# Optimization experiments

Measured on AMD Instinct MI355X. Metric: run time of the kernel, lower is better.

## Reference

```python
import jax, jax.numpy as jnp
import numpy as np

T_STEPS = 15
THR1, THR2 = 10.0, 1.0
KWTA2, RAD2 = 8, 1


def _conv(x, w):
    # x: [T, Cin, H, W] (time steps treated as batch), w: [Cout, Cin, kh, kw]
    return jax.lax.conv_general_dilated(
        x, w, window_strides=(1, 1), padding='VALID',
        dimension_numbers=('NCHW', 'OIHW', 'NCHW'))


def _fire(pot, thr):
    # torch threshold_(pot, thr, 0): keep values strictly > thr
    tp = jnp.where(pot > thr, pot, 0.0)
    return jnp.sign(tp), tp


def _max_pool(x, k, s, p):
    return jax.lax.reduce_window(
        x, -jnp.inf, jax.lax.max,
        window_dimensions=(1, 1, k, k), window_strides=(1, 1, s, s),
        padding=((0, 0), (0, 0), (p, p), (p, p)))


def _pointwise_inhibition(tp):
    # tp: [T, C, H, W] thresholded potentials. Keep, at each (h,w), only the
    # feature with the earliest spike (ties broken by max potential).
    T = tp.shape[0]
    max_val = jnp.max(tp, axis=1, keepdims=True)          # [T,1,H,W]
    max_idx = jnp.argmax(tp, axis=1, keepdims=True)       # [T,1,H,W]
    clamp = jnp.sign(max_val)                             # [T,1,H,W]
    earliest = jnp.clip(T - clamp.sum(axis=0, keepdims=True).astype(jnp.int32),
                        0, T - 1)                          # [1,1,H,W]
    winners = jnp.take_along_axis(max_idx, earliest, axis=0)  # [1,1,H,W]
    last_sign = clamp[-1:]                                 # [1,1,H,W]
    C = tp.shape[1]
    onehot = (jnp.arange(C)[None, :, None, None] == winners).astype(tp.dtype)
    coef = onehot * last_sign                              # [1,C,H,W]
    return tp * coef


def _get_k_winners(pot, spk, kwta, radius):
    # pot, spk: [T, C, H, W]
    T, C, H, W = pot.shape
    earliest = jnp.clip(T - spk.sum(axis=0, keepdims=True).astype(jnp.int32),
                        0, T - 1)                          # [1,C,H,W]
    values = jnp.take_along_axis(pot, earliest, axis=0)    # earliest potential
    trunc = spk * values
    v = trunc.max() * T
    total = (trunc + spk * v).sum(axis=0)                  # [C,H,W]
    c_idx = jnp.arange(C)[:, None, None]
    h_idx = jnp.arange(H)[None, :, None]
    w_idx = jnp.arange(W)[None, None, :]

    def step(tot, _):
        idx = jnp.argmax(tot.reshape(-1))
        mval = tot.reshape(-1)[idx]
        valid = mval != 0
        c = idx // (H * W)
        rem = idx % (H * W)
        h = rem // W
        w = rem % W
        # suppress the winning feature everywhere + columnar inhibition window
        mask = (c_idx == c) | ((jnp.abs(h_idx - h) <= radius) &
                               (jnp.abs(w_idx - w) <= radius))
        tot = jnp.where(valid & mask, 0.0, tot)
        winner = jnp.where(valid, jnp.stack([c, h, w]).astype(jnp.int32),
                           jnp.full((3,), -1, jnp.int32))
        return tot, winner

    _, winners = jax.lax.scan(step, total, None, length=kwta)
    return winners  # [kwta, 3], -1 rows = no winner


def setup_inputs() -> dict:
    key = jax.random.key(0)
    k1, k2, k3 = jax.random.split(key, 3)
    # cumulative spike-wave: once a pixel spikes it stays 1 for later timesteps
    u = jax.random.uniform(k1, (T_STEPS, 2, 192, 192), dtype=jnp.float32)
    x = jax.lax.cummax((u < 0.05).astype(jnp.float32), axis=0)
    w1 = 0.8 + 0.05 * jax.random.normal(k2, (32, 2, 5, 5), dtype=jnp.float32)
    w2 = 0.8 + 0.05 * jax.random.normal(k3, (150, 32, 2, 2), dtype=jnp.float32)
    return {"x": x, "w1": w1, "w2": w2}


def reference(x, w1, w2):
    # training path, layer_idx != 1 (trains conv2): exercises pooling,
    # pointwise inhibition, fire, and k-winner-take-all.
    xin = jnp.pad(x, ((0, 0), (0, 0), (2, 2), (2, 2)))
    pot1 = _conv(xin, w1)                     # [T,32,192,192]
    spk1, _ = _fire(pot1, THR1)
    spk_pool = _max_pool(spk1, 2, 2, 1)       # [T,32,97,97]
    spk_in = jnp.pad(spk_pool, ((0, 0), (0, 0), (1, 1), (1, 1)))
    spk_in = _pointwise_inhibition(spk_in)
    pot2 = _conv(spk_in, w2)                  # [T,150,98,98]
    _, tp2 = _fire(pot2, THR2)
    pot = _pointwise_inhibition(tp2)
    spk = jnp.sign(pot)
    winners = _get_k_winners(pot, spk, KWTA2, RAD2)
    return pot, winners
```

## Files before the change

### kernel.cpp

```cpp
#include <hip/hip_runtime.h>

#define NT 15
#define HW1 192
#define CIN 2
#define COUT1 32
#define PH 99
#define POOL 97
#define H2 98
#define COUT2 150
#define NLOC (H2 * H2)
#define POT_ELEMS 21609000
#define N4 5402256
#define CONV1_THREADS (1152 * 256)

typedef float f32x4 __attribute__((ext_vector_type(4)));

__global__ __launch_bounds__(256) void k_first_spike(const float* __restrict__ x,
                                                     unsigned char* __restrict__ tx) {
    const int N = CIN * HW1 * HW1;
    int i = blockIdx.x * 256 + threadIdx.x;
    if (i >= N) return;
    int t = 15;
    #pragma unroll
    for (int tt = NT - 1; tt >= 0; --tt) {
        if (x[tt * N + i] > 0.5f) t = tt;
    }
    tx[i] = (unsigned char)t;
}

__global__ __launch_bounds__(256) void k_conv1(const unsigned char* __restrict__ tx,
                                               const float* __restrict__ w1,
                                               unsigned char* __restrict__ t1,
                                               f32x4* __restrict__ outfill) {
    __shared__ unsigned char stx[CIN][20][20];
    const int by = blockIdx.y * 16, bx = blockIdx.x * 16;
    const int ocg = blockIdx.z * 4;
    const int tid = threadIdx.y * 16 + threadIdx.x;

    for (int i = tid; i < CIN * 400; i += 256) {
        int ic = i / 400, rem = i % 400, r = rem / 20, c = rem % 20;
        int gy = by + r - 2, gx = bx + c - 2;
        unsigned char v = 15;
        if (gy >= 0 && gy < HW1 && gx >= 0 && gx < HW1)
            v = tx[ic * (HW1 * HW1) + gy * HW1 + gx];
        stx[ic][r][c] = v;
    }
    __syncthreads();

    {
        int bid = (blockIdx.z * 12 + blockIdx.y) * 12 + blockIdx.x;
        int g = bid * 256 + tid;
        const f32x4 z = {0.0f, 0.0f, 0.0f, 0.0f};
        for (int i = g; i < N4; i += CONV1_THREADS)
            __builtin_nontemporal_store(z, &outfill[i]);
    }

    unsigned msk[50];
    #pragma unroll
    for (int ic = 0; ic < 2; ic++)
        #pragma unroll
        for (int ky = 0; ky < 5; ky++)
            #pragma unroll
            for (int kx = 0; kx < 5; kx++)
                msk[ic * 25 + ky * 5 + kx] =
                    0xFFFFFFFFu << stx[ic][threadIdx.y + ky][threadIdx.x + kx];

    const float* wbase = w1 + ocg * 50;
    int lo[4] = {0, 0, 0, 0};
    #pragma unroll
    for (int step = 8; step >= 1; step >>= 1) {
        #pragma unroll
        for (int o = 0; o < 4; o++) {
            int mid = lo[o] + step - 1;
            float acc = 0.0f;
            #pragma unroll
            for (int q = 0; q < 50; q++) {
                float b = (float)((msk[q] >> mid) & 1u);
                acc = fmaf(wbase[o * 50 + q], b, acc);
            }
            if (!(acc > 10.0f)) lo[o] += step;
        }
    }
    const int y = by + threadIdx.y, x = bx + threadIdx.x;
    #pragma unroll
    for (int o = 0; o < 4; o++)
        t1[(ocg + o) * (HW1 * HW1) + y * HW1 + x] = (unsigned char)lo[o];
}

__global__ __launch_bounds__(256) void k_pool_inhib1(const unsigned char* __restrict__ t1,
                                                     int* __restrict__ packed) {
    int i = blockIdx.x * 256 + threadIdx.x;
    if (i >= PH * PH) return;
    int ph = i / PH, pw = i % PH;
    int s = 15, c = 0;
    if (ph >= 1 && ph <= POOL && pw >= 1 && pw <= POOL) {
        int r0 = 2 * (ph - 1) - 1, c0 = 2 * (pw - 1) - 1;
        for (int oc = 0; oc < COUT1; ++oc) {
            int m = 15;
            #pragma unroll
            for (int dr = 0; dr < 2; dr++) {
                int rr = r0 + dr;
                if (rr < 0 || rr >= HW1) continue;
                #pragma unroll
                for (int dc = 0; dc < 2; dc++) {
                    int cc = c0 + dc;
                    if (cc < 0 || cc >= HW1) continue;
                    int v = t1[oc * (HW1 * HW1) + rr * HW1 + cc];
                    m = min(m, v);
                }
            }
            if (m < s) { s = m; c = oc; }
        }
    }
    packed[i] = (s << 8) | c;
}

__global__ __launch_bounds__(256) void k_transpose_w2(const float* __restrict__ w2,
                                                      float* __restrict__ w2t) {
    int i = blockIdx.x * 256 + threadIdx.x;
    if (i >= COUT2 * COUT1 * 4) return;
    int oc = i % COUT2;
    int ct = i / COUT2;
    int c = ct >> 2, tap = ct & 3;
    w2t[i] = w2[(oc * COUT1 + c) * 4 + tap];
}

__global__ __launch_bounds__(256) void k_conv2(const int* __restrict__ packed,
                                               const float* __restrict__ w2t,
                                               float* __restrict__ out,
                                               float* __restrict__ val1a,
                                               int* __restrict__ na,
                                               int* __restrict__ cwa) {
    int wid = threadIdx.x >> 6;
    int lane = threadIdx.x & 63;
    int loc = blockIdx.x * 4 + wid;
    if (loc >= NLOC) return;
    int y = loc / H2, x = loc % H2;
    int s[4], c[4];
    #pragma unroll
    for (int k = 0; k < 4; k++) {
        int p = packed[(y + (k >> 1)) * PH + (x + (k & 1))];
        s[k] = p >> 8; c[k] = p & 255;
    }
    float wv[3][4];
    int tmin = 15;
    #pragma unroll
    for (int r = 0; r < 3; r++) {
        int oc = lane + 64 * r;
        #pragma unroll
        for (int k = 0; k < 4; k++) wv[r][k] = 0.0f;
        if (oc < COUT2) {
            #pragma unroll
            for (int k = 0; k < 4; k++)
                if (s[k] < 15)
                    wv[r][k] = w2t[(c[k] * 4 + k) * COUT2 + oc];
            int tstar = 15;
            #pragma unroll
            for (int k = 0; k < 4; k++) {
                float sum = 0.0f;
                #pragma unroll
                for (int j = 0; j < 4; j++) sum += (s[j] <= s[k]) ? wv[r][j] : 0.0f;
                int cand = (sum > 1.0f && s[k] < 15) ? s[k] : 15;
                tstar = min(tstar, cand);
            }
            tmin = min(tmin, tstar);
        }
    }
    #pragma unroll
    for (int o = 32; o > 0; o >>= 1) tmin = min(tmin, __shfl_down(tmin, o));
    int earliest = __shfl(tmin, 0);
    if (earliest >= 15) {
        if (lane == 0) { val1a[loc] = 0.0f; na[loc] = 0; cwa[loc] = 0; }
        return;
    }
    float btp = 0.0f; int boc = 1 << 20;
    #pragma unroll
    for (int r = 0; r < 3; r++) {
        int oc = lane + 64 * r;
        if (oc < COUT2) {
            float v2 = 0.0f;
            #pragma unroll
            for (int j = 0; j < 4; j++) v2 += (s[j] <= earliest) ? wv[r][j] : 0.0f;
            float tp = (v2 > 1.0f) ? v2 : 0.0f;
            if (tp > btp || (tp == btp && oc < boc)) { btp = tp; boc = oc; }
        }
    }
    #pragma unroll
    for (int o = 32; o > 0; o >>= 1) {
        float ov = __shfl_down(btp, o);
        int oo = __shfl_down(boc, o);
        if (ov > btp || (ov == btp && oo < boc)) { btp = ov; boc = oo; }
    }
    btp = __shfl(btp, 0);
    boc = __shfl(boc, 0);
    int wr = boc >> 6, wl = boc & 63;
    if (lane == wl) {
        #pragma unroll
        for (int rr = 0; rr < 3; rr++) {
            if (rr == wr) {
                for (int t = earliest; t < 15; t++) {
                    float vv = 0.0f;
                    #pragma unroll
                    for (int j = 0; j < 4; j++) vv += (s[j] <= t) ? wv[rr][j] : 0.0f;
                    out[((t * COUT2 + boc) * H2 + y) * H2 + x] = vv;
                }
            }
        }
        val1a[loc] = btp;
        na[loc] = 15 - earliest;
        cwa[loc] = boc;
    }
}

__global__ __launch_bounds__(1024) void k_kwta(const float* __restrict__ val1a,
                                               const int* __restrict__ na,
                                               const int* __restrict__ cwa,
                                               float* __restrict__ out) {
    __shared__ float fred[16];
    __shared__ unsigned long long wred[16];
    int tid = threadIdx.x;
    float va[10];
    int nav[10], cwv[10], hwv[10];
    float lmax = 0.0f;
    #pragma unroll
    for (int j = 0; j < 10; j++) {
        int i = j * 1024 + tid;
        if (i < NLOC) {
            va[j] = val1a[i];
            nav[j] = na[i];
            cwv[j] = cwa[i];
            hwv[j] = ((i / H2) << 16) | (i % H2);
            lmax = fmaxf(lmax, va[j]);
        } else {
            va[j] = 0.0f; nav[j] = 0; cwv[j] = -2; hwv[j] = (1000 << 16) | 1000;
        }
    }
    #pragma unroll
    for (int o = 32; o > 0; o >>= 1) lmax = fmaxf(lmax, __shfl_xor(lmax, o));
    if ((tid & 63) == 0) fred[tid >> 6] = lmax;
    __syncthreads();
    float gmax = fred[0];
    #pragma unroll
    for (int wvi = 1; wvi < 16; wvi++) gmax = fmaxf(gmax, fred[wvi]);
    float v = gmax * 15.0f;

    unsigned long long key[10];
    #pragma unroll
    for (int j = 0; j < 10; j++) {
        int i = j * 1024 + tid;
        float e = va[j] + v;
        float ssum = 0.0f;
        for (int q = 0; q < nav[j]; q++) ssum += e;
        int fidx = cwv[j] * NLOC + i;
        key[j] = ((unsigned long long)__float_as_uint(ssum) << 32)
               | (unsigned)(0x7FFFFFFF - fidx);
        if (nav[j] == 0) key[j] &= 0xFFFFFFFFull;
    }
    for (int k = 0; k < 8; k++) {
        unsigned long long best = 0;
        #pragma unroll
        for (int j = 0; j < 10; j++) best = (key[j] > best) ? key[j] : best;
        #pragma unroll
        for (int o = 32; o > 0; o >>= 1) {
            unsigned long long ok = __shfl_xor(best, o);
            best = (ok > best) ? ok : best;
        }
        if ((tid & 63) == 0) wred[tid >> 6] = best;
        __syncthreads();
        unsigned long long g = wred[0];
        #pragma unroll
        for (int wvi = 1; wvi < 16; wvi++) {
            unsigned long long t = wred[wvi];
            g = (t > g) ? t : g;
        }
        __syncthreads();
        float mv = __uint_as_float((unsigned)(g >> 32));
        int fidx = 0x7FFFFFFF - (int)(unsigned)(g & 0xFFFFFFFFu);
        bool valid = (mv != 0.0f);
        int wc = fidx / NLOC;
        int rem = fidx - wc * NLOC;
        int wh = rem / H2, ww = rem - wh * H2;
        if (tid == 0) {
            out[POT_ELEMS + k * 3 + 0] = valid ? (float)wc : -1.0f;
            out[POT_ELEMS + k * 3 + 1] = valid ? (float)wh : -1.0f;
            out[POT_ELEMS + k * 3 + 2] = valid ? (float)ww : -1.0f;
        }
        if (valid) {
            #pragma unroll
            for (int j = 0; j < 10; j++) {
                int h = hwv[j] >> 16, w = hwv[j] & 0xFFFF;
                if (cwv[j] == wc || (abs(h - wh) <= 1 && abs(w - ww) <= 1))
                    key[j] &= 0xFFFFFFFFull;
            }
        }
    }
}

extern "C" void kernel_launch(void* const* d_in, const int* in_sizes, int n_in,
                              void* d_out, int out_size, void* d_ws, size_t ws_size,
                              hipStream_t stream) {
    const float* x  = (const float*)d_in[0];
    const float* w1 = (const float*)d_in[1];
    const float* w2 = (const float*)d_in[2];
    float* out = (float*)d_out;
    char* ws = (char*)d_ws;

    unsigned char* tx = (unsigned char*)ws;
    unsigned char* t1 = (unsigned char*)(ws + 73728);
    int*   packed = (int*)(ws + 1253376);
    float* val1a  = (float*)(ws + 1292580);
    int*   na     = (int*)(ws + 1330996);
    int*   cwa    = (int*)(ws + 1369412);
    float* w2t    = (float*)(ws + 1407840);

    k_first_spike<<<288, 256, 0, stream>>>(x, tx);
    k_conv1<<<dim3(12, 12, 8), dim3(16, 16), 0, stream>>>(tx, w1, t1, (f32x4*)d_out);
    k_pool_inhib1<<<(PH * PH + 255) / 256, 256, 0, stream>>>(t1, packed);
    k_transpose_w2<<<75, 256, 0, stream>>>(w2, w2t);
    k_conv2<<<(NLOC + 3) / 4, 256, 0, stream>>>(packed, w2t, out, val1a, na, cwa);
    k_kwta<<<1, 1024, 0, stream>>>(val1a, na, cwa, out);
}
```

Measured before the change: 106.2 us.

## Fuse first-spike into conv1, interleave output zero-fill, merge pool and weight transpose

Computes first-spike times directly inside conv1's shared-memory tile load instead of in a separate kernel. The output zero-fill stores are split into chunks interleaved with the binary-search threshold steps using scheduling barriers, so memory stores overlap compute. The w2 transpose is merged into the pooling/inhibition kernel. Together these remove two launches and an intermediate buffer, at the cost of redundant x reads across the channel-group blocks.

```diff
diff --git a/kernel.cpp b/kernel.cpp
--- a/kernel.cpp
+++ b/kernel.cpp
@@ -15,20 +15,7 @@
 
 typedef float f32x4 __attribute__((ext_vector_type(4)));
 
-__global__ __launch_bounds__(256) void k_first_spike(const float* __restrict__ x,
-                                                     unsigned char* __restrict__ tx) {
-    const int N = CIN * HW1 * HW1;
-    int i = blockIdx.x * 256 + threadIdx.x;
-    if (i >= N) return;
-    int t = 15;
-    #pragma unroll
-    for (int tt = NT - 1; tt >= 0; --tt) {
-        if (x[tt * N + i] > 0.5f) t = tt;
-    }
-    tx[i] = (unsigned char)t;
-}
-
-__global__ __launch_bounds__(256) void k_conv1(const unsigned char* __restrict__ tx,
+__global__ __launch_bounds__(256) void k_conv1(const float* __restrict__ x,
                                                const float* __restrict__ w1,
                                                unsigned char* __restrict__ t1,
                                                f32x4* __restrict__ outfill) {
@@ -36,24 +23,23 @@
     const int by = blockIdx.y * 16, bx = blockIdx.x * 16;
     const int ocg = blockIdx.z * 4;
     const int tid = threadIdx.y * 16 + threadIdx.x;
+    const int NPIX = HW1 * HW1;
 
     for (int i = tid; i < CIN * 400; i += 256) {
         int ic = i / 400, rem = i % 400, r = rem / 20, c = rem % 20;
         int gy = by + r - 2, gx = bx + c - 2;
         unsigned char v = 15;
-        if (gy >= 0 && gy < HW1 && gx >= 0 && gx < HW1)
-            v = tx[ic * (HW1 * HW1) + gy * HW1 + gx];
+        if (gy >= 0 && gy < HW1 && gx >= 0 && gx < HW1) {
+            const float* xp = x + ic * NPIX + gy * HW1 + gx;
+            int t = 15;
+            #pragma unroll
+            for (int tt = NT - 1; tt >= 0; --tt)
+                if (xp[tt * (CIN * NPIX)] > 0.5f) t = tt;
+            v = (unsigned char)t;
+        }
         stx[ic][r][c] = v;
     }
     __syncthreads();
-
-    {
-        int bid = (blockIdx.z * 12 + blockIdx.y) * 12 + blockIdx.x;
-        int g = bid * 256 + tid;
-        const f32x4 z = {0.0f, 0.0f, 0.0f, 0.0f};
-        for (int i = g; i < N4; i += CONV1_THREADS)
-            __builtin_nontemporal_store(z, &outfill[i]);
-    }
 
     unsigned msk[50];
     #pragma unroll
@@ -67,8 +53,18 @@
 
     const float* wbase = w1 + ocg * 50;
     int lo[4] = {0, 0, 0, 0};
-    #pragma unroll
-    for (int step = 8; step >= 1; step >>= 1) {
+    const int bid = (blockIdx.z * 12 + blockIdx.y) * 12 + blockIdx.x;
+    const int g = bid * 256 + tid;
+    const f32x4 z = {0.0f, 0.0f, 0.0f, 0.0f};
+
+    auto do_fill = [&](int k0, int k1) {
+        #pragma unroll
+        for (int k = k0; k < k1; k++) {
+            int i = g + k * CONV1_THREADS;
+            if (i < N4) __builtin_nontemporal_store(z, &outfill[i]);
+        }
+    };
+    auto do_step = [&](int step) {
         #pragma unroll
         for (int o = 0; o < 4; o++) {
             int mid = lo[o] + step - 1;
@@ -80,16 +76,35 @@
             }
             if (!(acc > 10.0f)) lo[o] += step;
         }
-    }
-    const int y = by + threadIdx.y, x = bx + threadIdx.x;
+    };
+
+    do_fill(0, 4);   __builtin_amdgcn_sched_barrier(0);
+    do_step(8);      __builtin_amdgcn_sched_barrier(0);
+    do_fill(4, 8);   __builtin_amdgcn_sched_barrier(0);
+    do_step(4);      __builtin_amdgcn_sched_barrier(0);
+    do_fill(8, 12);  __builtin_amdgcn_sched_barrier(0);
+    do_step(2);      __builtin_amdgcn_sched_barrier(0);
+    do_fill(12, 16); __builtin_amdgcn_sched_barrier(0);
+    do_step(1);      __builtin_amdgcn_sched_barrier(0);
+    do_fill(16, 19);
+
+    const int y = by + threadIdx.y, xx = bx + threadIdx.x;
     #pragma unroll
     for (int o = 0; o < 4; o++)
-        t1[(ocg + o) * (HW1 * HW1) + y * HW1 + x] = (unsigned char)lo[o];
-}
-
-__global__ __launch_bounds__(256) void k_pool_inhib1(const unsigned char* __restrict__ t1,
-                                                     int* __restrict__ packed) {
+        t1[(ocg + o) * NPIX + y * HW1 + xx] = (unsigned char)lo[o];
+}
+
+__global__ __launch_bounds__(256) void k_pool_tr(const unsigned char* __restrict__ t1,
+                                                 int* __restrict__ packed,
+                                                 const float* __restrict__ w2,
+                                                 float* __restrict__ w2t) {
     int i = blockIdx.x * 256 + threadIdx.x;
+    {
+        int oc = i % COUT2;
+        int ct = i / COUT2;
+        int c = ct >> 2, tap = ct & 3;
+        w2t[i] = w2[(oc * COUT1 + c) * 4 + tap];
+    }
     if (i >= PH * PH) return;
     int ph = i / PH, pw = i % PH;
     int s = 15, c = 0;
@@ -113,16 +128,6 @@
         }
     }
     packed[i] = (s << 8) | c;
-}
-
-__global__ __launch_bounds__(256) void k_transpose_w2(const float* __restrict__ w2,
-                                                      float* __restrict__ w2t) {
-    int i = blockIdx.x * 256 + threadIdx.x;
-    if (i >= COUT2 * COUT1 * 4) return;
-    int oc = i % COUT2;
-    int ct = i / COUT2;
-    int c = ct >> 2, tap = ct & 3;
-    w2t[i] = w2[(oc * COUT1 + c) * 4 + tap];
 }
 
 __global__ __launch_bounds__(256) void k_conv2(const int* __restrict__ packed,
@@ -305,7 +310,6 @@
     float* out = (float*)d_out;
     char* ws = (char*)d_ws;
 
-    unsigned char* tx = (unsigned char*)ws;
     unsigned char* t1 = (unsigned char*)(ws + 73728);
     int*   packed = (int*)(ws + 1253376);
     float* val1a  = (float*)(ws + 1292580);
@@ -313,10 +317,8 @@
     int*   cwa    = (int*)(ws + 1369412);
     float* w2t    = (float*)(ws + 1407840);
 
-    k_first_spike<<<288, 256, 0, stream>>>(x, tx);
-    k_conv1<<<dim3(12, 12, 8), dim3(16, 16), 0, stream>>>(tx, w1, t1, (f32x4*)d_out);
-    k_pool_inhib1<<<(PH * PH + 255) / 256, 256, 0, stream>>>(t1, packed);
-    k_transpose_w2<<<75, 256, 0, stream>>>(w2, w2t);
+    k_conv1<<<dim3(12, 12, 8), dim3(16, 16), 0, stream>>>(x, w1, t1, (f32x4*)d_out);
+    k_pool_tr<<<75, 256, 0, stream>>>(t1, packed, w2, w2t);
     k_conv2<<<(NLOC + 3) / 4, 256, 0, stream>>>(packed, w2t, out, val1a, na, cwa);
     k_kwta<<<1, 1024, 0, stream>>>(val1a, na, cwa, out);
 }
```

After: 123.1 us. 16.0% more time.

## Fuse w2 transpose into pooling kernel and process two locations per wave in conv2

Applied to the files above, without the earlier changes.

Merges the w2 transpose kernel into the pool/inhibition kernel, removing one launch. conv2 now handles two output locations per wavefront, halving the grid. The serial per-time-step potential write by a single lane becomes a parallel write across lanes, with the winner's weights broadcast by shuffles. The fused kernel relies on its 75 blocks exactly covering the 19200 weight elements, and the halved grid lowers the number of waves available to hide latency.

```diff
diff --git a/kernel.cpp b/kernel.cpp
--- a/kernel.cpp
+++ b/kernel.cpp
@@ -9,6 +9,7 @@
 #define H2 98
 #define COUT2 150
 #define NLOC (H2 * H2)
+#define HALF_LOC 4802
 #define POT_ELEMS 21609000
 #define N4 5402256
 #define CONV1_THREADS (1152 * 256)
@@ -87,9 +88,17 @@
         t1[(ocg + o) * (HW1 * HW1) + y * HW1 + x] = (unsigned char)lo[o];
 }
 
-__global__ __launch_bounds__(256) void k_pool_inhib1(const unsigned char* __restrict__ t1,
-                                                     int* __restrict__ packed) {
+__global__ __launch_bounds__(256) void k_pool_tr(const unsigned char* __restrict__ t1,
+                                                 int* __restrict__ packed,
+                                                 const float* __restrict__ w2,
+                                                 float* __restrict__ w2t) {
     int i = blockIdx.x * 256 + threadIdx.x;
+    {
+        int oc = i % COUT2;
+        int ct = i / COUT2;
+        int c = ct >> 2, tap = ct & 3;
+        w2t[i] = w2[(oc * COUT1 + c) * 4 + tap];
+    }
     if (i >= PH * PH) return;
     int ph = i / PH, pw = i % PH;
     int s = 15, c = 0;
@@ -115,16 +124,6 @@
     packed[i] = (s << 8) | c;
 }
 
-__global__ __launch_bounds__(256) void k_transpose_w2(const float* __restrict__ w2,
-                                                      float* __restrict__ w2t) {
-    int i = blockIdx.x * 256 + threadIdx.x;
-    if (i >= COUT2 * COUT1 * 4) return;
-    int oc = i % COUT2;
-    int ct = i / COUT2;
-    int c = ct >> 2, tap = ct & 3;
-    w2t[i] = w2[(oc * COUT1 + c) * 4 + tap];
-}
-
 __global__ __launch_bounds__(256) void k_conv2(const int* __restrict__ packed,
                                                const float* __restrict__ w2t,
                                                float* __restrict__ out,
@@ -133,82 +132,89 @@
                                                int* __restrict__ cwa) {
     int wid = threadIdx.x >> 6;
     int lane = threadIdx.x & 63;
-    int loc = blockIdx.x * 4 + wid;
-    if (loc >= NLOC) return;
-    int y = loc / H2, x = loc % H2;
-    int s[4], c[4];
-    #pragma unroll
-    for (int k = 0; k < 4; k++) {
-        int p = packed[(y + (k >> 1)) * PH + (x + (k & 1))];
-        s[k] = p >> 8; c[k] = p & 255;
-    }
-    float wv[3][4];
-    int tmin = 15;
-    #pragma unroll
-    for (int r = 0; r < 3; r++) {
-        int oc = lane + 64 * r;
-        #pragma unroll
-        for (int k = 0; k < 4; k++) wv[r][k] = 0.0f;
-        if (oc < COUT2) {
-            #pragma unroll
-            for (int k = 0; k < 4; k++)
-                if (s[k] < 15)
-                    wv[r][k] = w2t[(c[k] * 4 + k) * COUT2 + oc];
-            int tstar = 15;
-            #pragma unroll
-            for (int k = 0; k < 4; k++) {
-                float sum = 0.0f;
+    int W = blockIdx.x * 4 + wid;
+    if (W >= HALF_LOC) return;
+    #pragma unroll
+    for (int li = 0; li < 2; li++) {
+        int loc = W + li * HALF_LOC;
+        int y = loc / H2, x = loc % H2;
+        int s[4], c[4];
+        #pragma unroll
+        for (int k = 0; k < 4; k++) {
+            int p = packed[(y + (k >> 1)) * PH + (x + (k & 1))];
+            s[k] = p >> 8; c[k] = p & 255;
+        }
+        float wv[3][4];
+        int tmin = 15;
+        #pragma unroll
+        for (int r = 0; r < 3; r++) {
+            int oc = lane + 64 * r;
+            #pragma unroll
+            for (int k = 0; k < 4; k++) wv[r][k] = 0.0f;
+            if (oc < COUT2) {
                 #pragma unroll
-                for (int j = 0; j < 4; j++) sum += (s[j] <= s[k]) ? wv[r][j] : 0.0f;
-                int cand = (sum > 1.0f && s[k] < 15) ? s[k] : 15;
-                tstar = min(tstar, cand);
-            }
-            tmin = min(tmin, tstar);
-        }
-    }
-    #pragma unroll
-    for (int o = 32; o > 0; o >>= 1) tmin = min(tmin, __shfl_down(tmin, o));
-    int earliest = __shfl(tmin, 0);
-    if (earliest >= 15) {
-        if (lane == 0) { val1a[loc] = 0.0f; na[loc] = 0; cwa[loc] = 0; }
-        return;
-    }
-    float btp = 0.0f; int boc = 1 << 20;
-    #pragma unroll
-    for (int r = 0; r < 3; r++) {
-        int oc = lane + 64 * r;
-        if (oc < COUT2) {
-            float v2 = 0.0f;
-            #pragma unroll
-            for (int j = 0; j < 4; j++) v2 += (s[j] <= earliest) ? wv[r][j] : 0.0f;
-            float tp = (v2 > 1.0f) ? v2 : 0.0f;
-            if (tp > btp || (tp == btp && oc < boc)) { btp = tp; boc = oc; }
-        }
-    }
-    #pragma unroll
-    for (int o = 32; o > 0; o >>= 1) {
-        float ov = __shfl_down(btp, o);
-        int oo = __shfl_down(boc, o);
-        if (ov > btp || (ov == btp && oo < boc)) { btp = ov; boc = oo; }
-    }
-    btp = __shfl(btp, 0);
-    boc = __shfl(boc, 0);
-    int wr = boc >> 6, wl = boc & 63;
-    if (lane == wl) {
-        #pragma unroll
-        for (int rr = 0; rr < 3; rr++) {
-            if (rr == wr) {
-                for (int t = earliest; t < 15; t++) {
-                    float vv = 0.0f;
+                for (int k = 0; k < 4; k++)
+                    if (s[k] < 15)
+                        wv[r][k] = w2t[(c[k] * 4 + k) * COUT2 + oc];
+                int tstar = 15;
+                #pragma unroll
+                for (int k = 0; k < 4; k++) {
+                    float sum = 0.0f;
                     #pragma unroll
-                    for (int j = 0; j < 4; j++) vv += (s[j] <= t) ? wv[rr][j] : 0.0f;
-                    out[((t * COUT2 + boc) * H2 + y) * H2 + x] = vv;
+                    for (int j = 0; j < 4; j++) sum += (s[j] <= s[k]) ? wv[r][j] : 0.0f;
+                    int cand = (sum > 1.0f && s[k] < 15) ? s[k] : 15;
+                    tstar = min(tstar, cand);
                 }
-            }
-        }
-        val1a[loc] = btp;
-        na[loc] = 15 - earliest;
-        cwa[loc] = boc;
+                tmin = min(tmin, tstar);
+            }
+        }
+        #pragma unroll
+        for (int o = 32; o > 0; o >>= 1) tmin = min(tmin, __shfl_down(tmin, o));
+        int earliest = __shfl(tmin, 0);
+        if (earliest >= 15) {
+            if (lane == 0) { val1a[loc] = 0.0f; na[loc] = 0; cwa[loc] = 0; }
+            continue;
+        }
+        float btp = 0.0f; int boc = 1 << 20;
+        #pragma unroll
+        for (int r = 0; r < 3; r++) {
+            int oc = lane + 64 * r;
+            if (oc < COUT2) {
+                float v2 = 0.0f;
+                #pragma unroll
+                for (int j = 0; j < 4; j++) v2 += (s[j] <= earliest) ? wv[r][j] : 0.0f;
+                float tp = (v2 > 1.0f) ? v2 : 0.0f;
+                if (tp > btp || (tp == btp && oc < boc)) { btp = tp; boc = oc; }
+            }
+        }
+        #pragma unroll
+        for (int o = 32; o > 0; o >>= 1) {
+            float ov = __shfl_down(btp, o);
+            int oo = __shfl_down(boc, o);
+            if (ov > btp || (ov == btp && oo < boc)) { btp = ov; boc = oo; }
+        }
+        btp = __shfl(btp, 0);
+        boc = __shfl(boc, 0);
+        int wr = boc >> 6, wl = boc & 63;
+        float u0 = 0.0f, u1 = 0.0f, u2 = 0.0f, u3 = 0.0f;
+        #pragma unroll
+        for (int rr = 0; rr < 3; rr++)
+            if (rr == wr) { u0 = wv[rr][0]; u1 = wv[rr][1]; u2 = wv[rr][2]; u3 = wv[rr][3]; }
+        u0 = __shfl(u0, wl); u1 = __shfl(u1, wl); u2 = __shfl(u2, wl); u3 = __shfl(u3, wl);
+        if (lane >= earliest && lane < 15) {
+            int t = lane;
+            float vv = 0.0f;
+            vv += (s[0] <= t) ? u0 : 0.0f;
+            vv += (s[1] <= t) ? u1 : 0.0f;
+            vv += (s[2] <= t) ? u2 : 0.0f;
+            vv += (s[3] <= t) ? u3 : 0.0f;
+            out[((t * COUT2 + boc) * H2 + y) * H2 + x] = vv;
+        }
+        if (lane == 0) {
+            val1a[loc] = btp;
+            na[loc] = 15 - earliest;
+            cwa[loc] = boc;
+        }
     }
 }
 
@@ -315,8 +321,7 @@
 
     k_first_spike<<<288, 256, 0, stream>>>(x, tx);
     k_conv1<<<dim3(12, 12, 8), dim3(16, 16), 0, stream>>>(tx, w1, t1, (f32x4*)d_out);
-    k_pool_inhib1<<<(PH * PH + 255) / 256, 256, 0, stream>>>(t1, packed);
-    k_transpose_w2<<<75, 256, 0, stream>>>(w2, w2t);
-    k_conv2<<<(NLOC + 3) / 4, 256, 0, stream>>>(packed, w2t, out, val1a, na, cwa);
+    k_pool_tr<<<75, 256, 0, stream>>>(t1, packed, w2, w2t);
+    k_conv2<<<(HALF_LOC + 3) / 4, 256, 0, stream>>>(packed, w2t, out, val1a, na, cwa);
     k_kwta<<<1, 1024, 0, stream>>>(val1a, na, cwa, out);
 }
```

Measured after the change: 101.5 us. 4.4% less time.
